# Optimization experiments

Hardware: AMD Instinct MI355X
Metric: run time of the kernel (lower is better)

The kernel has to match this reference:

```python
import jax, jax.numpy as jnp
import numpy as np
from math import sqrt

D_MODEL = 1024
NUM_HEADS = 16
MASK_VAL = -100000000.0


def setup_inputs() -> dict:
    key = jax.random.key(0)
    k1, k2, k3, k4, k5 = jax.random.split(key, 5)
    scale = 1.0 / sqrt(D_MODEL)
    return {
        "in_features": jax.random.normal(k1, (2, 2048, D_MODEL), dtype=jnp.float32),
        "q_proj_weight": jax.random.normal(k2, (D_MODEL, D_MODEL), dtype=jnp.float32) * scale,
        "k_proj_weight": jax.random.normal(k3, (D_MODEL, D_MODEL), dtype=jnp.float32) * scale,
        "v_proj_weight": jax.random.normal(k4, (D_MODEL, D_MODEL), dtype=jnp.float32) * scale,
        "o_proj_weight": jax.random.normal(k5, (D_MODEL, D_MODEL), dtype=jnp.float32) * scale,
    }


def _proj_heads(x, w, h):
    # x: [b, s, d_in], w: [h*d, d_in] -> [b, h, s, d]
    d = w.shape[0] // h
    w = w.reshape(h, d, w.shape[1])
    return jnp.einsum('bsi,hdi->bhsd', x, w)


def reference(in_features, q_proj_weight, k_proj_weight, v_proj_weight, o_proj_weight):
    h = NUM_HEADS
    b, s, _ = in_features.shape
    q = _proj_heads(in_features, q_proj_weight, h)  # [b,h,s,dk]
    k = _proj_heads(in_features, k_proj_weight, h)
    v = _proj_heads(in_features, v_proj_weight, h)
    d_k = q.shape[-1]
    # additive causal mask: -1e8 above diagonal
    mask = jnp.triu(jnp.full((s, s), MASK_VAL, dtype=q.dtype), k=1)[None, None]
    scores = jnp.einsum('bhqd,bhkd->bhqk', q, k) / sqrt(d_k) + mask
    attn = jax.nn.softmax(scores, axis=-1)
    out = jnp.einsum('bhqk,bhkd->bhqd', attn, v)          # [b,h,s,dv]
    out = out.transpose(0, 2, 1, 3).reshape(b, s, -1)      # [b,s,h*dv]
    return jnp.einsum('bsv,mv->bsm', out, o_proj_weight)
```

## Files before the change

### kernel.cpp

```cpp
#include <hip/hip_runtime.h>
#include <hip/hip_bf16.h>
#include <stdint.h>
#include <type_traits>

typedef __bf16 bf16;
typedef __bf16 bf16x4 __attribute__((ext_vector_type(4)));
typedef __bf16 bf16x8 __attribute__((ext_vector_type(8)));
typedef float floatx4 __attribute__((ext_vector_type(4)));
typedef unsigned int u32;

#define D_MODEL 1024
#define SEQ 2048
#define NHEADS 16
#define DH 64
#define BATCH 2
#define MROWS (BATCH * SEQ)

#define XELEMS ((size_t)MROWS * D_MODEL)
#define WELEMS ((size_t)D_MODEL * D_MODEL)
#define CVT_ELEMS (XELEMS + 4 * WELEMS)

__device__ __forceinline__ void gload_lds16(const void* g, void* l) {
  __builtin_amdgcn_global_load_lds(
      (const __attribute__((address_space(1))) u32*)g,
      (__attribute__((address_space(3))) u32*)l, 16, 0, 0);
}

__global__ __launch_bounds__(256) void cvt_f32_bf16(
    const float* __restrict__ s0, const float* __restrict__ s1,
    const float* __restrict__ s2, const float* __restrict__ s3,
    const float* __restrict__ s4, bf16* __restrict__ dst) {
  const size_t i = ((size_t)blockIdx.x * 256 + threadIdx.x) * 8;
  const float* src;
  size_t off;
  if (i < XELEMS) {
    src = s0; off = i;
  } else {
    const size_t j = i - XELEMS;
    const int r = (int)(j / WELEMS);
    src = (r == 0) ? s1 : (r == 1) ? s2 : (r == 2) ? s3 : s4;
    off = j - (size_t)r * WELEMS;
  }
  floatx4 f0 = *(const floatx4*)&src[off];
  floatx4 f1 = *(const floatx4*)&src[off + 4];
  bf16x8 o;
#pragma unroll
  for (int j = 0; j < 4; j++) { o[j] = (bf16)f0[j]; o[4 + j] = (bf16)f1[j]; }
  *(bf16x8*)&dst[i] = o;
}

__global__ __launch_bounds__(256) void gemm_qkv(
    const bf16* __restrict__ A, const bf16* __restrict__ Wq,
    const bf16* __restrict__ Wk, const bf16* __restrict__ Wv,
    bf16* __restrict__ Qo, bf16* __restrict__ Ko, bf16* __restrict__ Vto) {
  const int z = blockIdx.z;
  const bf16* W = (z == 0) ? Wq : (z == 1) ? Wk : Wv;

  __shared__ bf16 As[128 * 64];
  __shared__ bf16 Bs[128 * 64];

  const int tid = threadIdx.x;
  const int lane = tid & 63;
  const int w = tid >> 6;
  const int lo16 = lane & 15;
  const int quad = lane >> 4;
  const int wy = w >> 1, wx = w & 1;

  const int m0 = blockIdx.y * 128;
  const int n0 = blockIdx.x * 128;

  const int sl = lane >> 3;
  const int sc = ((lane & 7) ^ sl) * 8;

  const floatx4 fz = {0.f, 0.f, 0.f, 0.f};
  floatx4 acc[4][4];
#pragma unroll
  for (int i = 0; i < 4; i++)
#pragma unroll
    for (int j = 0; j < 4; j++) acc[i][j] = fz;

  auto kloop = [&](auto vt) {
    constexpr bool VT = decltype(vt)::value;
    for (int k0 = 0; k0 < 1024; k0 += 64) {
      __syncthreads();
#pragma unroll
      for (int i = 0; i < 4; i++) {
        const int seg = i * 4 + w;
        const int row = seg * 8 + sl;
        gload_lds16(&A[(size_t)(m0 + row) * 1024 + k0 + sc], &As[seg * 512]);
        gload_lds16(&W[(size_t)(n0 + row) * 1024 + k0 + sc], &Bs[seg * 512]);
      }
      __syncthreads();

#pragma unroll
      for (int kk = 0; kk < 64; kk += 32) {
        bf16x8 af[4], bfr[4];
        const int cc = (kk >> 3) + quad;
#pragma unroll
        for (int t = 0; t < 4; t++) {
          const int ra = wy * 64 + t * 16 + lo16;
          const int rb = wx * 64 + t * 16 + lo16;
          af[t]  = *(const bf16x8*)&As[ra * 64 + ((cc ^ (ra & 7)) << 3)];
          bfr[t] = *(const bf16x8*)&Bs[rb * 64 + ((cc ^ (rb & 7)) << 3)];
        }
#pragma unroll
        for (int mt = 0; mt < 4; mt++)
#pragma unroll
          for (int nt = 0; nt < 4; nt++) {
            if constexpr (VT)
              acc[mt][nt] = __builtin_amdgcn_mfma_f32_16x16x32_bf16(bfr[nt], af[mt], acc[mt][nt], 0, 0, 0);
            else
              acc[mt][nt] = __builtin_amdgcn_mfma_f32_16x16x32_bf16(af[mt], bfr[nt], acc[mt][nt], 0, 0, 0);
          }
      }
    }
  };
  if (z == 2) kloop(std::true_type{}); else kloop(std::false_type{});

  if (z < 2) {
    bf16* C = (z == 0) ? Qo : Ko;
#pragma unroll
    for (int mt = 0; mt < 4; mt++)
#pragma unroll
      for (int nt = 0; nt < 4; nt++)
#pragma unroll
        for (int r = 0; r < 4; r++) {
          const int row = m0 + wy * 64 + mt * 16 + quad * 4 + r;
          const int col = n0 + wx * 64 + nt * 16 + lo16;
          C[(size_t)row * D_MODEL + col] = (bf16)acc[mt][nt][r];
        }
  } else {
#pragma unroll
    for (int mt = 0; mt < 4; mt++)
#pragma unroll
      for (int nt = 0; nt < 4; nt++)
#pragma unroll
        for (int r = 0; r < 4; r++) {
          const int feat = n0 + wx * 64 + nt * 16 + quad * 4 + r;
          const int tok  = m0 + wy * 64 + mt * 16 + lo16;
          const int hh = feat >> 6, dd = feat & 63;
          const int bb = tok >> 11, ss = tok & 2047;
          Vto[(size_t)((bb * NHEADS + hh) * DH + dd) * SEQ + ss] = (bf16)acc[mt][nt][r];
        }
  }
}

__global__ __launch_bounds__(256) void gemm_o(
    const bf16* __restrict__ A, const bf16* __restrict__ W,
    float* __restrict__ C) {
  __shared__ bf16 As[2 * 64 * 64];
  __shared__ bf16 Bs[2 * 128 * 64];

  const int tid = threadIdx.x;
  const int lane = tid & 63;
  const int w = tid >> 6;
  const int lo16 = lane & 15;
  const int quad = lane >> 4;
  const int wy = w >> 1, wx = w & 1;

  const int m0 = blockIdx.y * 64;
  const int n0 = blockIdx.x * 128;

  const int sl = lane >> 3;
  const int sc = ((lane & 7) ^ sl) * 8;

  const floatx4 fz = {0.f, 0.f, 0.f, 0.f};
  floatx4 acc[2][4];
#pragma unroll
  for (int i = 0; i < 2; i++)
#pragma unroll
    for (int j = 0; j < 4; j++) acc[i][j] = fz;

  for (int k0 = 0; k0 < 1024; k0 += 128) {
    __syncthreads();
#pragma unroll
    for (int kh = 0; kh < 2; kh++) {
#pragma unroll
      for (int i = 0; i < 2; i++) {
        const int seg = i * 4 + w;
        const int row = seg * 8 + sl;
        gload_lds16(&A[(size_t)(m0 + row) * 1024 + k0 + kh * 64 + sc],
                    &As[kh * 4096 + seg * 512]);
      }
#pragma unroll
      for (int i = 0; i < 4; i++) {
        const int seg = i * 4 + w;
        const int row = seg * 8 + sl;
        gload_lds16(&W[(size_t)(n0 + row) * 1024 + k0 + kh * 64 + sc],
                    &Bs[kh * 8192 + seg * 512]);
      }
    }
    __syncthreads();

#pragma unroll
    for (int kk = 0; kk < 128; kk += 32) {
      const int kh = kk >> 6;
      const int cc = ((kk & 63) >> 3) + quad;
      bf16x8 af[2], bfr[4];
#pragma unroll
      for (int t = 0; t < 2; t++) {
        const int ra = wy * 32 + t * 16 + lo16;
        af[t] = *(const bf16x8*)&As[kh * 4096 + ra * 64 + ((cc ^ (ra & 7)) << 3)];
      }
#pragma unroll
      for (int t = 0; t < 4; t++) {
        const int rb = wx * 64 + t * 16 + lo16;
        bfr[t] = *(const bf16x8*)&Bs[kh * 8192 + rb * 64 + ((cc ^ (rb & 7)) << 3)];
      }
#pragma unroll
      for (int mt = 0; mt < 2; mt++)
#pragma unroll
        for (int nt = 0; nt < 4; nt++)
          acc[mt][nt] = __builtin_amdgcn_mfma_f32_16x16x32_bf16(af[mt], bfr[nt], acc[mt][nt], 0, 0, 0);
    }
  }

#pragma unroll
  for (int mt = 0; mt < 2; mt++)
#pragma unroll
    for (int nt = 0; nt < 4; nt++)
#pragma unroll
      for (int r = 0; r < 4; r++) {
        const int row = m0 + wy * 32 + mt * 16 + quad * 4 + r;
        const int col = n0 + wx * 64 + nt * 16 + lo16;
        C[(size_t)row * D_MODEL + col] = acc[mt][nt][r];
      }
}

#define LPK 72
#define LPV 136
#define LPP 72

__global__ __launch_bounds__(512, 4) void attn_causal(
    const bf16* __restrict__ Q, const bf16* __restrict__ Kg,
    const bf16* __restrict__ Vt, bf16* __restrict__ O) {
  __shared__ __align__(16) char smem[54272];
  bf16* Ks  = (bf16*)smem;
  bf16* VTs = (bf16*)(smem + 18432);
  bf16* Ps  = (bf16*)(smem + 35840);
  float* Es = (float*)smem;

  const int tid = threadIdx.x;
  const int lane = tid & 63;
  const int wid = tid >> 6;
  const int g = wid >> 2;
  const int w4 = wid & 3;
  const int lo16 = lane & 15;
  const int quad = lane >> 4;

  const int x = blockIdx.x;
  const int qtA = x;
  const int qtB = 31 - x;
  const int nA = (qtA + 2) >> 1;
  const int nB = (qtB + 2) >> 1;
  const int h = blockIdx.y;
  const int b = blockIdx.z;
  const size_t base  = (size_t)b * SEQ * D_MODEL + (size_t)h * DH;
  const size_t baset = (size_t)(b * NHEADS + h) * DH * SEQ;

  const int rA = qtA * 64 + w4 * 16 + lo16;
  const int rB = qtB * 64 + w4 * 16 + lo16;
  bf16x8 qfA[2], qfB[2];
#pragma unroll
  for (int ks = 0; ks < 2; ks++) {
    qfA[ks] = *(const bf16x8*)&Q[base + (size_t)rA * D_MODEL + ks * 32 + quad * 8];
    qfB[ks] = *(const bf16x8*)&Q[base + (size_t)rB * D_MODEL + ks * 32 + quad * 8];
  }

  bf16x8 onesf;
#pragma unroll
  for (int j = 0; j < 8; j++) onesf[j] = (bf16)1.0f;

  const floatx4 fz = {0.f, 0.f, 0.f, 0.f};
  floatx4 oA[4], oB[4];
  floatx4 lA = fz, lB = fz;
#pragma unroll
  for (int i = 0; i < 4; i++) { oA[i] = fz; oB[i] = fz; }

  const int kr = tid >> 3;
  const int kc = (tid & 7) * 8;

  bf16x8 kvp[2], vvp[2];
#pragma unroll
  for (int c2 = 0; c2 < 2; c2++) {
    kvp[c2] = *(const bf16x8*)&Kg[base + (size_t)(c2 * 64 + kr) * D_MODEL + kc];
    vvp[c2] = *(const bf16x8*)&Vt[baset + (size_t)kr * SEQ + c2 * 64 + kc];
  }

  for (int c = 0; c < nB; c++) {
    const int j0 = c * 128;
    __syncthreads();
#pragma unroll
    for (int c2 = 0; c2 < 2; c2++) {
      *(bf16x8*)&Ks[(c2 * 64 + kr) * LPK + kc] = kvp[c2];
      *(bf16x8*)&VTs[kr * LPV + c2 * 64 + kc] = vvp[c2];
    }
    __syncthreads();

    if (c + 1 < nB) {
      const int j1 = j0 + 128;
#pragma unroll
      for (int c2 = 0; c2 < 2; c2++) {
        kvp[c2] = *(const bf16x8*)&Kg[base + (size_t)(j1 + c2 * 64 + kr) * D_MODEL + kc];
        vvp[c2] = *(const bf16x8*)&Vt[baset + (size_t)kr * SEQ + j1 + c2 * 64 + kc];
      }
    }

    auto compute = [&](int q0s, const bf16x8* qf, floatx4* oacc, floatx4& lacc,
                       bool diag) {
      floatx4 sacc[4];
#pragma unroll
      for (int n = 0; n < 4; n++) sacc[n] = fz;
#pragma unroll
      for (int n = 0; n < 4; n++) {
        const int rk = g * 64 + n * 16 + lo16;
#pragma unroll
        for (int ks = 0; ks < 2; ks++) {
          bf16x8 kf = *(const bf16x8*)&Ks[rk * LPK + ks * 32 + quad * 8];
          sacc[n] = __builtin_amdgcn_mfma_f32_16x16x32_bf16(kf, qf[ks], sacc[n], 0, 0, 0);
        }
      }

      if (diag) {
        const int myq = q0s + w4 * 16 + lo16;
#pragma unroll
        for (int n = 0; n < 4; n++) {
          const int kvb = j0 + g * 64 + n * 16 + quad * 4;
          bf16x4 pk;
#pragma unroll
          for (int r = 0; r < 4; r++) {
            const float e = __builtin_amdgcn_exp2f(fmaf(sacc[n][r], 0.18033688f, -17.3123405f));
            pk[r] = (bf16)((kvb + r > myq) ? 0.f : e);
          }
          *(bf16x4*)&Ps[wid * 1152 + lo16 * LPP + n * 16 + quad * 4] = pk;
        }
      } else {
#pragma unroll
        for (int n = 0; n < 4; n++) {
          bf16x4 pk;
#pragma unroll
          for (int r = 0; r < 4; r++)
            pk[r] = (bf16)__builtin_amdgcn_exp2f(fmaf(sacc[n][r], 0.18033688f, -17.3123405f));
          *(bf16x4*)&Ps[wid * 1152 + lo16 * LPP + n * 16 + quad * 4] = pk;
        }
      }

#pragma unroll
      for (int ks = 0; ks < 2; ks++) {
        bf16x8 pf = *(const bf16x8*)&Ps[wid * 1152 + lo16 * LPP + ks * 32 + quad * 8];
#pragma unroll
        for (int dt = 0; dt < 4; dt++) {
          bf16x8 vf = *(const bf16x8*)&VTs[(dt * 16 + lo16) * LPV + g * 64 + ks * 32 + quad * 8];
          oacc[dt] = __builtin_amdgcn_mfma_f32_16x16x32_bf16(pf, vf, oacc[dt], 0, 0, 0);
        }
        lacc = __builtin_amdgcn_mfma_f32_16x16x32_bf16(pf, onesf, lacc, 0, 0, 0);
      }
    };

    compute(qtB * 64, qfB, oB, lB, c == nB - 1);
    if (c < nA) compute(qtA * 64, qfA, oA, lA, c == nA - 1);
  }

  __syncthreads();
  if (g == 1) {
    float* e = &Es[(w4 * 64 + lane) * 40];
#pragma unroll
    for (int dt = 0; dt < 4; dt++)
#pragma unroll
      for (int r = 0; r < 4; r++) e[dt * 4 + r] = oA[dt][r];
#pragma unroll
    for (int r = 0; r < 4; r++) e[16 + r] = lA[r];
#pragma unroll
    for (int dt = 0; dt < 4; dt++)
#pragma unroll
      for (int r = 0; r < 4; r++) e[20 + dt * 4 + r] = oB[dt][r];
#pragma unroll
    for (int r = 0; r < 4; r++) e[36 + r] = lB[r];
  }
  __syncthreads();
  if (g == 0) {
    const float* e = &Es[(w4 * 64 + lane) * 40];
#pragma unroll
    for (int dt = 0; dt < 4; dt++)
#pragma unroll
      for (int r = 0; r < 4; r++) { oA[dt][r] += e[dt * 4 + r]; oB[dt][r] += e[20 + dt * 4 + r]; }
#pragma unroll
    for (int r = 0; r < 4; r++) { lA[r] += e[16 + r]; lB[r] += e[36 + r]; }

    auto finish = [&](int q0s, floatx4* oacc, floatx4 lacc) {
#pragma unroll
      for (int r = 0; r < 4; r++) {
        const float inv = 1.0f / lacc[r];
        const int row = q0s + w4 * 16 + quad * 4 + r;
#pragma unroll
        for (int dt = 0; dt < 4; dt++)
          O[base + (size_t)row * D_MODEL + dt * 16 + lo16] = (bf16)(oacc[dt][r] * inv);
      }
    };
    finish(qtA * 64, oA, lA);
    finish(qtB * 64, oB, lB);
  }
}

extern "C" void kernel_launch(void* const* d_in, const int* in_sizes, int n_in,
                              void* d_out, int out_size, void* d_ws, size_t ws_size,
                              hipStream_t stream) {
  const float* X  = (const float*)d_in[0];
  const float* Wq = (const float*)d_in[1];
  const float* Wk = (const float*)d_in[2];
  const float* Wv = (const float*)d_in[3];
  const float* Wo = (const float*)d_in[4];
  float* out = (float*)d_out;

  bf16* cvt = (bf16*)d_ws;
  bf16* Xb  = cvt;
  bf16* Wqb = cvt + XELEMS;
  bf16* Wkb = Wqb + WELEMS;
  bf16* Wvb = Wkb + WELEMS;
  bf16* Wob = Wvb + WELEMS;
  bf16* Qb  = cvt + CVT_ELEMS;
  bf16* Kb  = Qb + XELEMS;
  bf16* Vtb = Kb + XELEMS;
  bf16* Ob  = Vtb + XELEMS;

  dim3 blk(256);
  cvt_f32_bf16<<<dim3((u32)(CVT_ELEMS / (256 * 8))), blk, 0, stream>>>(
      X, Wq, Wk, Wv, Wo, cvt);
  gemm_qkv<<<dim3(8, 32, 3), blk, 0, stream>>>(Xb, Wqb, Wkb, Wvb, Qb, Kb, Vtb);
  attn_causal<<<dim3(16, NHEADS, BATCH), dim3(512), 0, stream>>>(Qb, Kb, Vtb, Ob);
  gemm_o<<<dim3(8, 64), blk, 0, stream>>>(Ob, Wob, out);
}
```

Baseline: 177.5 us.

## Triple-buffer QKV GEMM with 256x128 tiles and 512-thread blocks

Reworks the fused QKV projection GEMM to use a three-stage LDS ring, so global-to-LDS loads for tile t+2 are issued before computing tile t, with vmcnt-based waits replacing the double syncthreads. Block tiles grow to 256 rows with 8 waves, so the 128-column weight tile is shared by twice as many rows. The three weight matrices are treated as one contiguous 3072-row weight on a 2D grid. The price is more LDS per block (about 144 KB), which lowers occupancy and fragility from hand-counted vmcnt values.

After: 168.5 us. 5.1% less time.

```diff
diff --git a/kernel.cpp b/kernel.cpp
--- a/kernel.cpp
+++ b/kernel.cpp
@@ -49,25 +49,24 @@
   *(bf16x8*)&dst[i] = o;
 }
 
-__global__ __launch_bounds__(256) void gemm_qkv(
-    const bf16* __restrict__ A, const bf16* __restrict__ Wq,
-    const bf16* __restrict__ Wk, const bf16* __restrict__ Wv,
+#define QKV_ASLOT (256 * 64)
+#define QKV_SLOT  (256 * 64 + 128 * 64)
+
+__global__ __launch_bounds__(512) void gemm_qkv(
+    const bf16* __restrict__ A, const bf16* __restrict__ W,
     bf16* __restrict__ Qo, bf16* __restrict__ Ko, bf16* __restrict__ Vto) {
-  const int z = blockIdx.z;
-  const bf16* W = (z == 0) ? Wq : (z == 1) ? Wk : Wv;
-
-  __shared__ bf16 As[128 * 64];
-  __shared__ bf16 Bs[128 * 64];
+  __shared__ bf16 sm[3 * QKV_SLOT];
 
   const int tid = threadIdx.x;
   const int lane = tid & 63;
   const int w = tid >> 6;
   const int lo16 = lane & 15;
   const int quad = lane >> 4;
-  const int wy = w >> 1, wx = w & 1;
-
-  const int m0 = blockIdx.y * 128;
+  const int wy = w >> 1;
+  const int wx = w & 1;
+
   const int n0 = blockIdx.x * 128;
+  const int m0 = blockIdx.y * 256;
 
   const int sl = lane >> 3;
   const int sc = ((lane & 7) ^ sl) * 8;
@@ -79,46 +78,78 @@
 #pragma unroll
     for (int j = 0; j < 4; j++) acc[i][j] = fz;
 
-  auto kloop = [&](auto vt) {
+  auto stage = [&](int t, int s) {
+    bf16* As = &sm[s * QKV_SLOT];
+    bf16* Bs = As + QKV_ASLOT;
+    const int k0 = t * 64;
+#pragma unroll
+    for (int i = 0; i < 4; i++) {
+      const int seg = w * 4 + i;
+      const int row = seg * 8 + sl;
+      gload_lds16(&A[(size_t)(m0 + row) * 1024 + k0 + sc], &As[seg * 512]);
+    }
+#pragma unroll
+    for (int i = 0; i < 2; i++) {
+      const int seg = w * 2 + i;
+      const int row = seg * 8 + sl;
+      gload_lds16(&W[(size_t)(n0 + row) * 1024 + k0 + sc], &Bs[seg * 512]);
+    }
+  };
+
+  auto compute = [&](int s, auto vt) {
     constexpr bool VT = decltype(vt)::value;
-    for (int k0 = 0; k0 < 1024; k0 += 64) {
-      __syncthreads();
-#pragma unroll
-      for (int i = 0; i < 4; i++) {
-        const int seg = i * 4 + w;
-        const int row = seg * 8 + sl;
-        gload_lds16(&A[(size_t)(m0 + row) * 1024 + k0 + sc], &As[seg * 512]);
-        gload_lds16(&W[(size_t)(n0 + row) * 1024 + k0 + sc], &Bs[seg * 512]);
-      }
-      __syncthreads();
-
-#pragma unroll
-      for (int kk = 0; kk < 64; kk += 32) {
-        bf16x8 af[4], bfr[4];
-        const int cc = (kk >> 3) + quad;
-#pragma unroll
-        for (int t = 0; t < 4; t++) {
-          const int ra = wy * 64 + t * 16 + lo16;
-          const int rb = wx * 64 + t * 16 + lo16;
-          af[t]  = *(const bf16x8*)&As[ra * 64 + ((cc ^ (ra & 7)) << 3)];
-          bfr[t] = *(const bf16x8*)&Bs[rb * 64 + ((cc ^ (rb & 7)) << 3)];
-        }
-#pragma unroll
-        for (int mt = 0; mt < 4; mt++)
-#pragma unroll
-          for (int nt = 0; nt < 4; nt++) {
-            if constexpr (VT)
-              acc[mt][nt] = __builtin_amdgcn_mfma_f32_16x16x32_bf16(bfr[nt], af[mt], acc[mt][nt], 0, 0, 0);
-            else
-              acc[mt][nt] = __builtin_amdgcn_mfma_f32_16x16x32_bf16(af[mt], bfr[nt], acc[mt][nt], 0, 0, 0);
-          }
-      }
+    const bf16* As = &sm[s * QKV_SLOT];
+    const bf16* Bs = As + QKV_ASLOT;
+#pragma unroll
+    for (int kk = 0; kk < 64; kk += 32) {
+      bf16x8 af[4], bfr[4];
+      const int cc = (kk >> 3) + quad;
+#pragma unroll
+      for (int t = 0; t < 4; t++) {
+        const int ra = wy * 64 + t * 16 + lo16;
+        const int rb = wx * 64 + t * 16 + lo16;
+        af[t]  = *(const bf16x8*)&As[ra * 64 + ((cc ^ (ra & 7)) << 3)];
+        bfr[t] = *(const bf16x8*)&Bs[rb * 64 + ((cc ^ (rb & 7)) << 3)];
+      }
+#pragma unroll
+      for (int mt = 0; mt < 4; mt++)
+#pragma unroll
+        for (int nt = 0; nt < 4; nt++) {
+          if constexpr (VT)
+            acc[mt][nt] = __builtin_amdgcn_mfma_f32_16x16x32_bf16(bfr[nt], af[mt], acc[mt][nt], 0, 0, 0);
+          else
+            acc[mt][nt] = __builtin_amdgcn_mfma_f32_16x16x32_bf16(af[mt], bfr[nt], acc[mt][nt], 0, 0, 0);
+        }
     }
   };
-  if (z == 2) kloop(std::true_type{}); else kloop(std::false_type{});
-
-  if (z < 2) {
-    bf16* C = (z == 0) ? Qo : Ko;
+
+  auto step = [&](int t, int s, auto vt) {
+    if (t + 2 < 16) stage(t + 2, (t + 2) % 3);
+    compute(s, vt);
+    if (t < 15) {
+      if (t + 2 < 16) { asm volatile("s_waitcnt vmcnt(6)" ::: "memory"); }
+      else            { asm volatile("s_waitcnt vmcnt(0)" ::: "memory"); }
+      __builtin_amdgcn_s_barrier();
+    }
+  };
+
+  auto mainloop = [&](auto vt) {
+    stage(0, 0);
+    stage(1, 1);
+    asm volatile("s_waitcnt vmcnt(6)" ::: "memory");
+    __builtin_amdgcn_s_barrier();
+    for (int tb = 0; tb < 15; tb += 3) {
+      step(tb + 0, 0, vt);
+      step(tb + 1, 1, vt);
+      step(tb + 2, 2, vt);
+    }
+    step(15, 0, vt);
+  };
+  if (n0 >= 2048) mainloop(std::true_type{}); else mainloop(std::false_type{});
+
+  if (n0 < 2048) {
+    bf16* C = (n0 < 1024) ? Qo : Ko;
+    const int nc = (n0 < 1024) ? n0 : n0 - 1024;
 #pragma unroll
     for (int mt = 0; mt < 4; mt++)
 #pragma unroll
@@ -126,17 +157,18 @@
 #pragma unroll
         for (int r = 0; r < 4; r++) {
           const int row = m0 + wy * 64 + mt * 16 + quad * 4 + r;
-          const int col = n0 + wx * 64 + nt * 16 + lo16;
+          const int col = nc + wx * 64 + nt * 16 + lo16;
           C[(size_t)row * D_MODEL + col] = (bf16)acc[mt][nt][r];
         }
   } else {
+    const int nv = n0 - 2048;
 #pragma unroll
     for (int mt = 0; mt < 4; mt++)
 #pragma unroll
       for (int nt = 0; nt < 4; nt++)
 #pragma unroll
         for (int r = 0; r < 4; r++) {
-          const int feat = n0 + wx * 64 + nt * 16 + quad * 4 + r;
+          const int feat = nv + wx * 64 + nt * 16 + quad * 4 + r;
           const int tok  = m0 + wy * 64 + mt * 16 + lo16;
           const int hh = feat >> 6, dd = feat & 63;
           const int bb = tok >> 11, ss = tok & 2047;
@@ -415,9 +447,7 @@
   bf16* cvt = (bf16*)d_ws;
   bf16* Xb  = cvt;
   bf16* Wqb = cvt + XELEMS;
-  bf16* Wkb = Wqb + WELEMS;
-  bf16* Wvb = Wkb + WELEMS;
-  bf16* Wob = Wvb + WELEMS;
+  bf16* Wob = Wqb + 3 * WELEMS;
   bf16* Qb  = cvt + CVT_ELEMS;
   bf16* Kb  = Qb + XELEMS;
   bf16* Vtb = Kb + XELEMS;
@@ -426,7 +456,7 @@
   dim3 blk(256);
   cvt_f32_bf16<<<dim3((u32)(CVT_ELEMS / (256 * 8))), blk, 0, stream>>>(
       X, Wq, Wk, Wv, Wo, cvt);
-  gemm_qkv<<<dim3(8, 32, 3), blk, 0, stream>>>(Xb, Wqb, Wkb, Wvb, Qb, Kb, Vtb);
+  gemm_qkv<<<dim3(24, 16), dim3(512), 0, stream>>>(Xb, Wqb, Qb, Kb, Vtb);
   attn_causal<<<dim3(16, NHEADS, BATCH), dim3(512), 0, stream>>>(Qb, Kb, Vtb, Ob);
   gemm_o<<<dim3(8, 64), blk, 0, stream>>>(Ob, Wob, out);
 }
```
